# Optimization experiments

Measured on AMD Instinct MI355X. Metric: run time of the kernel, lower is better.

## Reference

```python
import math
import jax, jax.numpy as jnp
import numpy as np

B, L, D = 1, 2048, 3072
H, KV, HD = 32, 32, 96
THETA = 10000.0
MAXP, ORIGP = 131072, 4096
ROPE_SCALE = math.sqrt(1.0 + math.log(MAXP / ORIGP) / math.log(ORIGP))
ATTN_SCALE = HD ** -0.5
OP = H * HD + 2 * KV * HD  # 9216


def setup_inputs() -> dict:
    key = jax.random.key(0)
    k1, k2, k3, k4 = jax.random.split(key, 4)
    return {
        "x": jax.random.normal(k1, (B, L, D), jnp.float32),
        "w_qkv": jax.random.normal(k2, (OP, D), jnp.float32) * (D ** -0.5),
        "w_o": jax.random.normal(k3, (D, H * HD), jnp.float32) * ((H * HD) ** -0.5),
        # Phi-3 su-scaling short factors are ~1.0; sample near 1
        "short_factor": 1.0 + 0.5 * jax.random.uniform(k4, (HD // 2,), jnp.float32),
    }


def _rotate_half(t):
    t1, t2 = jnp.split(t, 2, axis=-1)
    return jnp.concatenate([-t2, t1], axis=-1)


def reference(x, w_qkv, w_o, short_factor):
    # fused QKV projection
    qkv = x @ w_qkv.T  # [B,L,OP]
    q, k, v = jnp.split(qkv, [H * HD, H * HD + KV * HD], axis=-1)
    q = q.reshape(B, L, H, HD).transpose(0, 2, 1, 3)   # [B,H,L,HD]
    k = k.reshape(B, L, KV, HD).transpose(0, 2, 1, 3)  # [B,KV,L,HD]
    v = v.reshape(B, L, KV, HD).transpose(0, 2, 1, 3)

    # SuRoPE (always uses short_factor, matching source)
    pos = jnp.arange(L, dtype=jnp.float32)  # position_ids default arange
    inv_freq = 1.0 / (short_factor * THETA ** (jnp.arange(0, HD, 2, dtype=jnp.float32) / HD))  # [HD/2]
    freqs = pos[:, None] * inv_freq[None, :]            # [L,HD/2]
    emb = jnp.concatenate([freqs, freqs], axis=-1)      # [L,HD]
    cos = (jnp.cos(emb) * ROPE_SCALE)[None, None]       # [1,1,L,HD]
    sin = (jnp.sin(emb) * ROPE_SCALE)[None, None]
    q = q * cos + _rotate_half(q) * sin
    k = k * cos + _rotate_half(k) * sin

    # causal mask, naive attention (matches source)
    mask = jnp.triu(jnp.full((L, L), -jnp.inf, dtype=jnp.float32), 1)
    scores = jnp.einsum('bhqd,bhkd->bhqk', q * ATTN_SCALE, k) + mask
    attn = jax.nn.softmax(scores, axis=-1)
    o = jnp.einsum('bhqk,bhkd->bhqd', attn, v)
    o = o.transpose(0, 2, 1, 3).reshape(B, L, H * HD)
    return o @ w_o.T
```

## Files before the change

kernel.cpp:

```cpp
#include <hip/hip_runtime.h>
#include <math.h>

typedef __attribute__((ext_vector_type(4))) float f32x4;
typedef __attribute__((ext_vector_type(4))) float f4;
typedef __attribute__((ext_vector_type(8))) _Float16 h8;
typedef __attribute__((ext_vector_type(8))) unsigned short us8;

static __device__ __forceinline__ h8 ld8h(const _Float16* p) {
    return __builtin_bit_cast(h8, *(const us8*)p);
}
static __device__ __forceinline__ void glds16(const void* g, void* l) {
    __builtin_amdgcn_global_load_lds((const __attribute__((address_space(1))) unsigned int*)g,
                                     (__attribute__((address_space(3))) unsigned int*)l, 16, 0, 0);
}

__global__ void convert_half(const float* __restrict__ in, _Float16* __restrict__ out, int n8) {
    int i = blockIdx.x * blockDim.x + threadIdx.x;
    if (i >= n8) return;
    f4 v0 = *(const f4*)(in + (size_t)i * 8);
    f4 v1 = *(const f4*)(in + (size_t)i * 8 + 4);
    h8 o;
#pragma unroll
    for (int j = 0; j < 4; j++) {
        o[j] = (_Float16)v0[j];
        o[j + 4] = (_Float16)v1[j];
    }
    *(h8*)(out + (size_t)i * 8) = o;
}

__global__ void rope_table(const float* __restrict__ sf, float* __restrict__ cs,
                           float* __restrict__ sn, float rope_scale) {
    int i = blockIdx.x * blockDim.x + threadIdx.x;
    const int j = i % 48, l = i / 48;
    const float e = (float)(2 * j) / 96.0f;
    const float inv = 1.0f / (sf[j] * powf(10000.0f, e));
    const float ang = (float)l * inv;
    cs[i] = cosf(ang) * rope_scale;
    sn[i] = sinf(ang) * rope_scale;
}

__global__ __launch_bounds__(256, 3) void gemm_qkv(
    const _Float16* __restrict__ A, const _Float16* __restrict__ B,
    const float* __restrict__ cs, const float* __restrict__ sn,
    _Float16* __restrict__ Qh, _Float16* __restrict__ Kh, _Float16* __restrict__ Vh,
    float attn_scale) {
    const int K = 3072;
    __shared__ _Float16 As[2][128][32], Bs[2][192][32];
    const int t = threadIdx.x;
    const int lane = t & 63, w = t >> 6;
    const int bm = blockIdx.y * 128, bn = blockIdx.x * 192;
    const int wm = w >> 1, wn = w & 1;
    const int l15 = lane & 15, l4 = lane >> 4;

    int car[2], cas[2], cbr[3], cbs[3];
#pragma unroll
    for (int i = 0; i < 2; i++) {
        const int c = t + i * 256;
        car[i] = c >> 2;
        cas[i] = (((c & 3) ^ ((car[i] >> 1) & 3)) * 8);
    }
#pragma unroll
    for (int i = 0; i < 3; i++) {
        const int c = t + i * 256;
        cbr[i] = c >> 2;
        cbs[i] = (((c & 3) ^ ((cbr[i] >> 1) & 3)) * 8);
    }

    f32x4 acc[4][6] = {};

#define STG_QKV(k0_, buf)                                                              \
    {                                                                                  \
        _Float16* ab = &As[(buf)][0][0];                                               \
        _Float16* bb = &Bs[(buf)][0][0];                                               \
        _Pragma("unroll") for (int i = 0; i < 2; i++)                                  \
            glds16(A + (size_t)(bm + car[i]) * K + (k0_) + cas[i], ab + (t + i * 256) * 8); \
        _Pragma("unroll") for (int i = 0; i < 3; i++)                                  \
            glds16(B + (size_t)(bn + cbr[i]) * K + (k0_) + cbs[i], bb + (t + i * 256) * 8); \
    }

    STG_QKV(0, 0)

    int cur = 0;
    for (int k0 = 0; k0 < K; k0 += 32) {
        __syncthreads();
        if (k0 + 32 < K) STG_QKV(k0 + 32, cur ^ 1)
        h8 af[4], bf[6];
#pragma unroll
        for (int m = 0; m < 4; m++) {
            const int row = wm * 64 + m * 16 + l15;
            af[m] = ld8h(&As[cur][row][(l4 ^ ((row >> 1) & 3)) * 8]);
        }
#pragma unroll
        for (int n = 0; n < 6; n++) {
            const int row = wn * 96 + n * 16 + l15;
            bf[n] = ld8h(&Bs[cur][row][(l4 ^ ((row >> 1) & 3)) * 8]);
        }
#pragma unroll
        for (int m = 0; m < 4; m++)
#pragma unroll
            for (int n = 0; n < 6; n++)
                acc[m][n] = __builtin_amdgcn_mfma_f32_16x16x32_f16(af[m], bf[n], acc[m][n], 0, 0, 0);
        cur ^= 1;
    }
#undef STG_QKV

    const int opcol0 = bn + wn * 96;
    const int which = opcol0 / 3072;
    const int h = (opcol0 % 3072) / 96;

    if (which == 2) {
#pragma unroll
        for (int m = 0; m < 4; m++)
#pragma unroll
            for (int r = 0; r < 4; r++) {
                const int l = bm + wm * 64 + m * 16 + l4 * 4 + r;
#pragma unroll
                for (int n = 0; n < 6; n++)
                    Vh[((size_t)h * 2048 + l) * 96 + n * 16 + l15] = (_Float16)acc[m][n][r];
            }
    } else {
        _Float16* dst = (which == 0) ? Qh : Kh;
        const float qs = (which == 0) ? attn_scale : 1.0f;
#pragma unroll
        for (int m = 0; m < 4; m++)
#pragma unroll
            for (int r = 0; r < 4; r++) {
                const int l = bm + wm * 64 + m * 16 + l4 * 4 + r;
                const float* csl = cs + l * 48;
                const float* snl = sn + l * 48;
                const size_t rowb = ((size_t)h * 2048 + l) * 96;
#pragma unroll
                for (int n = 0; n < 3; n++) {
                    const int j = n * 16 + l15;
                    const float c = csl[j], s = snl[j];
                    const float lo = acc[m][n][r], hi = acc[m][n + 3][r];
                    dst[rowb + j] = (_Float16)((lo * c - hi * s) * qs);
                    dst[rowb + j + 48] = (_Float16)((hi * c + lo * s) * qs);
                }
            }
    }
}

__global__ __launch_bounds__(256, 3) void gemm_p(
    const _Float16* __restrict__ A, const _Float16* __restrict__ B,
    float* __restrict__ C, int M, int N, int K) {
    __shared__ _Float16 As[2][128][32], Bs[2][96][32];
    const int t = threadIdx.x;
    const int lane = t & 63, w = t >> 6;
    const int bm = blockIdx.y * 128, bn = blockIdx.x * 96;
    const int wy = w >> 1, wx = w & 1;
    const int l15 = lane & 15, l4 = lane >> 4;

    int car[2], cas[2];
#pragma unroll
    for (int i = 0; i < 2; i++) {
        const int c = t + i * 256;
        car[i] = c >> 2;
        cas[i] = (((c & 3) ^ ((car[i] >> 1) & 3)) * 8);
    }
    const int cb0 = t, rb0 = cb0 >> 2, sb0 = (((cb0 & 3) ^ ((rb0 >> 1) & 3)) * 8);
    const int cb1 = t + 256, rb1 = cb1 >> 2, sb1 = (((cb1 & 3) ^ ((rb1 >> 1) & 3)) * 8);
    const bool bex = (t < 128);

    f32x4 acc[4][3] = {};

#define STG_P(k0_, buf)                                                                \
    {                                                                                  \
        _Float16* ab = &As[(buf)][0][0];                                               \
        _Float16* bb = &Bs[(buf)][0][0];                                               \
        _Pragma("unroll") for (int i = 0; i < 2; i++)                                  \
            glds16(A + (size_t)(bm + car[i]) * K + (k0_) + cas[i], ab + (t + i * 256) * 8); \
        glds16(B + (size_t)(bn + rb0) * K + (k0_) + sb0, bb + cb0 * 8);                \
        if (bex) glds16(B + (size_t)(bn + rb1) * K + (k0_) + sb1, bb + cb1 * 8);       \
    }

    STG_P(0, 0)

    int cur = 0;
    for (int k0 = 0; k0 < K; k0 += 32) {
        __syncthreads();
        if (k0 + 32 < K) STG_P(k0 + 32, cur ^ 1)
        h8 af[4], bf[3];
#pragma unroll
        for (int m = 0; m < 4; m++) {
            const int row = wy * 64 + m * 16 + l15;
            af[m] = ld8h(&As[cur][row][(l4 ^ ((row >> 1) & 3)) * 8]);
        }
#pragma unroll
        for (int n = 0; n < 3; n++) {
            const int row = wx * 48 + n * 16 + l15;
            bf[n] = ld8h(&Bs[cur][row][(l4 ^ ((row >> 1) & 3)) * 8]);
        }
#pragma unroll
        for (int m = 0; m < 4; m++)
#pragma unroll
            for (int n = 0; n < 3; n++)
                acc[m][n] = __builtin_amdgcn_mfma_f32_16x16x32_f16(af[m], bf[n], acc[m][n], 0, 0, 0);
        cur ^= 1;
    }
#undef STG_P

#pragma unroll
    for (int m = 0; m < 4; m++)
#pragma unroll
        for (int n = 0; n < 3; n++)
#pragma unroll
            for (int r = 0; r < 4; r++)
                C[(size_t)(bm + wy * 64 + m * 16 + l4 * 4 + r) * N + bn + wx * 48 + n * 16 + l15] =
                    acc[m][n][r];
}

__global__ __launch_bounds__(256) void vtrans(const _Float16* __restrict__ Vh,
                                              _Float16* __restrict__ Vt) {
    __shared__ _Float16 tile[64][105];
    const int h = blockIdx.y;
    const int l0 = blockIdx.x * 64;
    const int t = threadIdx.x;
#pragma unroll
    for (int i = 0; i < 3; i++) {
        const int v = t + i * 256;
        const int row = v / 12, seg = (v % 12) * 8;
        *(us8*)&tile[row][seg] =
            *(const us8*)(Vh + ((size_t)h * 2048 + l0 + row) * 96 + seg);
    }
    __syncthreads();
#pragma unroll
    for (int i = 0; i < 3; i++) {
        const int v = t + i * 256;
        const int d = v >> 3, lc = v & 7;
        h8 o;
#pragma unroll
        for (int j = 0; j < 8; j++) o[j] = tile[lc * 8 + j][d];
        *(h8*)(Vt + ((size_t)h * 96 + d) * 2048 + l0 + lc * 8) = o;
    }
}

__global__ __launch_bounds__(512, 2) void attn_mfma(
    const _Float16* __restrict__ Qh, const _Float16* __restrict__ Kh,
    const _Float16* __restrict__ Vt, _Float16* __restrict__ Oh) {
    __shared__ _Float16 Ks[2][64][104];
    __shared__ _Float16 Vs[2][96][72];
    __shared__ _Float16 Ps[8][16][72];

    const int h = blockIdx.y;
    const int t = threadIdx.x, lane = t & 63, w = t >> 6;
    const int l15 = lane & 15, l4 = lane >> 4;

    const _Float16* Kg = Kh + (size_t)h * 2048 * 96;
    const _Float16* Vg = Vt + (size_t)h * 96 * 2048;

    const int cA = t, rKA = cA / 12, sKA = (cA % 12) * 8;
    const int rVA = cA >> 3, sVA = (cA & 7) * 8;
    const int cB = 512 + t, rKB = cB / 12, sKB = (cB % 12) * 8;
    const int rVB = cB >> 3, sVB = (cB & 7) * 8;
    const bool two = (t < 256);

    for (int ph = 0; ph < 2; ph++) {
        const int qt = ph ? (int)blockIdx.x : 15 - (int)blockIdx.x;
        const int q0 = qt * 128;
        const int wq = q0 + w * 16;

        h8 qf[3];
        const size_t qrow = ((size_t)h * 2048 + wq + l15) * 96;
#pragma unroll
        for (int kc = 0; kc < 3; kc++) qf[kc] = ld8h(Qh + qrow + kc * 32 + l4 * 8);

        us8 kregA, vregA, kregB, vregB;
        kregA = *(const us8*)(Kg + (size_t)rKA * 96 + sKA);
        vregA = *(const us8*)(Vg + (size_t)rVA * 2048 + sVA);
        if (two) {
            kregB = *(const us8*)(Kg + (size_t)rKB * 96 + sKB);
            vregB = *(const us8*)(Vg + (size_t)rVB * 2048 + sVB);
        }

        f32x4 o[6] = {};
        float m_i[4] = {-1e30f, -1e30f, -1e30f, -1e30f};
        float l_i[4] = {0.f, 0.f, 0.f, 0.f};

        const int nkt = 2 * qt + 2;
        for (int kt = 0; kt < nkt; kt++) {
            const int kv0 = kt * 64;
            const int buf = kt & 1;
            *(us8*)&Ks[buf][rKA][sKA] = kregA;
            *(us8*)&Vs[buf][rVA][sVA] = vregA;
            if (two) {
                *(us8*)&Ks[buf][rKB][sKB] = kregB;
                *(us8*)&Vs[buf][rVB][sVB] = vregB;
            }
            __syncthreads();
            if (kt + 1 < nkt) {
                const int kv1 = kv0 + 64;
                kregA = *(const us8*)(Kg + (size_t)(kv1 + rKA) * 96 + sKA);
                vregA = *(const us8*)(Vg + (size_t)rVA * 2048 + kv1 + sVA);
                if (two) {
                    kregB = *(const us8*)(Kg + (size_t)(kv1 + rKB) * 96 + sKB);
                    vregB = *(const us8*)(Vg + (size_t)rVB * 2048 + kv1 + sVB);
                }
            }

            if (kv0 <= wq + 15) {
                f32x4 s[4] = {};
#pragma unroll
                for (int f = 0; f < 4; f++)
#pragma unroll
                    for (int kc = 0; kc < 3; kc++) {
                        h8 kf = ld8h(&Ks[buf][f * 16 + l15][kc * 32 + l4 * 8]);
                        s[f] = __builtin_amdgcn_mfma_f32_16x16x32_f16(qf[kc], kf, s[f], 0, 0, 0);
                    }

                if (kv0 + 63 > wq) {
#pragma unroll
                    for (int f = 0; f < 4; f++)
#pragma unroll
                        for (int r = 0; r < 4; r++)
                            if (kv0 + f * 16 + l15 > wq + l4 * 4 + r) s[f][r] = -1e30f;
                }

                float mx[4];
#pragma unroll
                for (int r = 0; r < 4; r++) {
                    float m0 = fmaxf(fmaxf(s[0][r], s[1][r]), fmaxf(s[2][r], s[3][r]));
#pragma unroll
                    for (int msk = 1; msk < 16; msk <<= 1) m0 = fmaxf(m0, __shfl_xor(m0, msk, 64));
                    mx[r] = m0;
                }

                bool need = false;
#pragma unroll
                for (int r = 0; r < 4; r++) need = need || (mx[r] > m_i[r] + 8.0f);
                if (__any(need)) {
#pragma unroll
                    for (int r = 0; r < 4; r++) {
                        const float mnew = fmaxf(m_i[r], mx[r]);
                        const float sc = __expf(m_i[r] - mnew);
                        m_i[r] = mnew;
                        l_i[r] *= sc;
#pragma unroll
                        for (int f2 = 0; f2 < 6; f2++) o[f2][r] *= sc;
                    }
                }

#pragma unroll
                for (int f = 0; f < 4; f++)
#pragma unroll
                    for (int r = 0; r < 4; r++) {
                        const float p = __expf(s[f][r] - m_i[r]);
                        Ps[w][l4 * 4 + r][f * 16 + l15] = (_Float16)p;
                        l_i[r] += p;
                    }
#pragma unroll
                for (int kc2 = 0; kc2 < 2; kc2++) {
                    h8 pa = ld8h(&Ps[w][l15][kc2 * 32 + l4 * 8]);
#pragma unroll
                    for (int f2 = 0; f2 < 6; f2++) {
                        h8 vb = ld8h(&Vs[buf][f2 * 16 + l15][kc2 * 32 + l4 * 8]);
                        o[f2] = __builtin_amdgcn_mfma_f32_16x16x32_f16(pa, vb, o[f2], 0, 0, 0);
                    }
                }
            }
        }

        __syncthreads();

#pragma unroll
        for (int r = 0; r < 4; r++) {
            float ss = l_i[r];
#pragma unroll
            for (int msk = 1; msk < 16; msk <<= 1) ss += __shfl_xor(ss, msk, 64);
            const float inv = 1.0f / ss;
            const size_t row = (size_t)(wq + l4 * 4 + r) * 3072 + h * 96;
#pragma unroll
            for (int f2 = 0; f2 < 6; f2++)
                Oh[row + f2 * 16 + l15] = (_Float16)(o[f2][r] * inv);
        }
    }
}

extern "C" void kernel_launch(void* const* d_in, const int* in_sizes, int n_in,
                              void* d_out, int out_size, void* d_ws, size_t ws_size,
                              hipStream_t stream) {
    const float* x = (const float*)d_in[0];
    const float* w_qkv = (const float*)d_in[1];
    const float* w_o = (const float*)d_in[2];
    const float* sf = (const float*)d_in[3];
    float* out = (float*)d_out;
    char* ws = (char*)d_ws;

    _Float16* wqkvh = (_Float16*)(ws);
    _Float16* Qh = (_Float16*)(ws + 56623104);
    _Float16* Kh = (_Float16*)(ws + 69206016);
    _Float16* Vh = (_Float16*)(ws + 81788928);
    _Float16* Vth = (_Float16*)(ws + 94371840);
    _Float16* Oh = (_Float16*)(ws + 106954752);
    _Float16* xh = (_Float16*)(ws + 132120576);
    _Float16* woh = (_Float16*)(ws + 144703488);
    float* cs = (float*)(ws + 163577856);
    float* sn = (float*)(ws + 163971072);

    const float rope_scale = (float)sqrt(1.0 + log(131072.0 / 4096.0) / log(4096.0));
    const float attn_scale = (float)(1.0 / sqrt(96.0));

    convert_half<<<3072, 256, 0, stream>>>(x, xh, 786432);
    convert_half<<<13824, 256, 0, stream>>>(w_qkv, wqkvh, 3538944);
    rope_table<<<384, 256, 0, stream>>>(sf, cs, sn, rope_scale);
    gemm_qkv<<<dim3(48, 16), 256, 0, stream>>>(xh, wqkvh, cs, sn, Qh, Kh, Vh, attn_scale);
    vtrans<<<dim3(32, 32), 256, 0, stream>>>(Vh, Vth);
    convert_half<<<4608, 256, 0, stream>>>(w_o, woh, 1179648);
    attn_mfma<<<dim3(8, 32), 512, 0, stream>>>(Qh, Kh, Vth, Oh);
    gemm_p<<<dim3(32, 16), 256, 0, stream>>>(Oh, woh, out, 2048, 3072, 3072);
}
```

Baseline: 317.6 us.

## Process two 16-row query groups per wave in attention, halving block size

The attention kernel now uses 256-thread blocks where each wave owns 32 query rows (two 16-row groups) instead of 16. Each K fragment and V fragment loaded from shared memory is reused for both groups' MFMAs, which cuts LDS reads per MFMA. V fragments are hoisted into registers before the softmax. The cost is more register pressure (two sets of accumulators, scores and Q fragments) and fewer waves per block for latency hiding, with the same total 512 blocks of work arranged over fewer threads.

New measurement: 345.0 us. 1.09x slower.

```diff
diff --git a/kernel.cpp b/kernel.cpp
--- a/kernel.cpp
+++ b/kernel.cpp
@@ -235,12 +235,12 @@
     }
 }
 
-__global__ __launch_bounds__(512, 2) void attn_mfma(
+__global__ __launch_bounds__(256, 2) void attn_mfma(
     const _Float16* __restrict__ Qh, const _Float16* __restrict__ Kh,
     const _Float16* __restrict__ Vt, _Float16* __restrict__ Oh) {
     __shared__ _Float16 Ks[2][64][104];
     __shared__ _Float16 Vs[2][96][72];
-    __shared__ _Float16 Ps[8][16][72];
+    __shared__ _Float16 Ps[4][16][72];
 
     const int h = blockIdx.y;
     const int t = threadIdx.x, lane = t & 63, w = t >> 6;
@@ -249,130 +249,155 @@
     const _Float16* Kg = Kh + (size_t)h * 2048 * 96;
     const _Float16* Vg = Vt + (size_t)h * 96 * 2048;
 
-    const int cA = t, rKA = cA / 12, sKA = (cA % 12) * 8;
-    const int rVA = cA >> 3, sVA = (cA & 7) * 8;
-    const int cB = 512 + t, rKB = cB / 12, sKB = (cB % 12) * 8;
-    const int rVB = cB >> 3, sVB = (cB & 7) * 8;
-    const bool two = (t < 256);
+    int rK[3], sK[3], rV[3], sV[3];
+#pragma unroll
+    for (int i = 0; i < 3; i++) {
+        const int c = t + i * 256;
+        rK[i] = c / 12; sK[i] = (c % 12) * 8;
+        rV[i] = c >> 3; sV[i] = (c & 7) * 8;
+    }
 
     for (int ph = 0; ph < 2; ph++) {
         const int qt = ph ? (int)blockIdx.x : 15 - (int)blockIdx.x;
         const int q0 = qt * 128;
-        const int wq = q0 + w * 16;
-
-        h8 qf[3];
-        const size_t qrow = ((size_t)h * 2048 + wq + l15) * 96;
-#pragma unroll
-        for (int kc = 0; kc < 3; kc++) qf[kc] = ld8h(Qh + qrow + kc * 32 + l4 * 8);
-
-        us8 kregA, vregA, kregB, vregB;
-        kregA = *(const us8*)(Kg + (size_t)rKA * 96 + sKA);
-        vregA = *(const us8*)(Vg + (size_t)rVA * 2048 + sVA);
-        if (two) {
-            kregB = *(const us8*)(Kg + (size_t)rKB * 96 + sKB);
-            vregB = *(const us8*)(Vg + (size_t)rVB * 2048 + sVB);
-        }
-
-        f32x4 o[6] = {};
-        float m_i[4] = {-1e30f, -1e30f, -1e30f, -1e30f};
-        float l_i[4] = {0.f, 0.f, 0.f, 0.f};
+        const int wq = q0 + w * 32;
+
+        h8 qf[2][3];
+#pragma unroll
+        for (int g = 0; g < 2; g++) {
+            const size_t qrow = ((size_t)h * 2048 + wq + g * 16 + l15) * 96;
+#pragma unroll
+            for (int kc = 0; kc < 3; kc++) qf[g][kc] = ld8h(Qh + qrow + kc * 32 + l4 * 8);
+        }
+
+        us8 kreg[3], vreg[3];
+#pragma unroll
+        for (int i = 0; i < 3; i++) {
+            kreg[i] = *(const us8*)(Kg + (size_t)rK[i] * 96 + sK[i]);
+            vreg[i] = *(const us8*)(Vg + (size_t)rV[i] * 2048 + sV[i]);
+        }
+
+        f32x4 o[2][6] = {};
+        float m_i[2][4], l_i[2][4];
+#pragma unroll
+        for (int g = 0; g < 2; g++)
+#pragma unroll
+            for (int r = 0; r < 4; r++) { m_i[g][r] = -1e30f; l_i[g][r] = 0.f; }
 
         const int nkt = 2 * qt + 2;
         for (int kt = 0; kt < nkt; kt++) {
             const int kv0 = kt * 64;
             const int buf = kt & 1;
-            *(us8*)&Ks[buf][rKA][sKA] = kregA;
-            *(us8*)&Vs[buf][rVA][sVA] = vregA;
-            if (two) {
-                *(us8*)&Ks[buf][rKB][sKB] = kregB;
-                *(us8*)&Vs[buf][rVB][sVB] = vregB;
+#pragma unroll
+            for (int i = 0; i < 3; i++) {
+                *(us8*)&Ks[buf][rK[i]][sK[i]] = kreg[i];
+                *(us8*)&Vs[buf][rV[i]][sV[i]] = vreg[i];
             }
             __syncthreads();
             if (kt + 1 < nkt) {
                 const int kv1 = kv0 + 64;
-                kregA = *(const us8*)(Kg + (size_t)(kv1 + rKA) * 96 + sKA);
-                vregA = *(const us8*)(Vg + (size_t)rVA * 2048 + kv1 + sVA);
-                if (two) {
-                    kregB = *(const us8*)(Kg + (size_t)(kv1 + rKB) * 96 + sKB);
-                    vregB = *(const us8*)(Vg + (size_t)rVB * 2048 + kv1 + sVB);
+#pragma unroll
+                for (int i = 0; i < 3; i++) {
+                    kreg[i] = *(const us8*)(Kg + (size_t)(kv1 + rK[i]) * 96 + sK[i]);
+                    vreg[i] = *(const us8*)(Vg + (size_t)rV[i] * 2048 + kv1 + sV[i]);
                 }
             }
 
-            if (kv0 <= wq + 15) {
-                f32x4 s[4] = {};
+            if (kv0 <= wq + 31) {
+                f32x4 s[2][4] = {};
 #pragma unroll
                 for (int f = 0; f < 4; f++)
 #pragma unroll
                     for (int kc = 0; kc < 3; kc++) {
                         h8 kf = ld8h(&Ks[buf][f * 16 + l15][kc * 32 + l4 * 8]);
-                        s[f] = __builtin_amdgcn_mfma_f32_16x16x32_f16(qf[kc], kf, s[f], 0, 0, 0);
+#pragma unroll
+                        for (int g = 0; g < 2; g++)
+                            s[g][f] = __builtin_amdgcn_mfma_f32_16x16x32_f16(qf[g][kc], kf, s[g][f], 0, 0, 0);
                     }
 
                 if (kv0 + 63 > wq) {
 #pragma unroll
+                    for (int g = 0; g < 2; g++)
+#pragma unroll
+                        for (int f = 0; f < 4; f++)
+#pragma unroll
+                            for (int r = 0; r < 4; r++)
+                                if (kv0 + f * 16 + l15 > wq + g * 16 + l4 * 4 + r) s[g][f][r] = -1e30f;
+                }
+
+                h8 vb[2][6];
+#pragma unroll
+                for (int kc2 = 0; kc2 < 2; kc2++)
+#pragma unroll
+                    for (int f2 = 0; f2 < 6; f2++)
+                        vb[kc2][f2] = ld8h(&Vs[buf][f2 * 16 + l15][kc2 * 32 + l4 * 8]);
+
+                float mx[2][4];
+#pragma unroll
+                for (int g = 0; g < 2; g++)
+#pragma unroll
+                    for (int r = 0; r < 4; r++) {
+                        float m0 = fmaxf(fmaxf(s[g][0][r], s[g][1][r]), fmaxf(s[g][2][r], s[g][3][r]));
+#pragma unroll
+                        for (int msk = 1; msk < 16; msk <<= 1) m0 = fmaxf(m0, __shfl_xor(m0, msk, 64));
+                        mx[g][r] = m0;
+                    }
+
+                bool need = false;
+#pragma unroll
+                for (int g = 0; g < 2; g++)
+#pragma unroll
+                    for (int r = 0; r < 4; r++) need = need || (mx[g][r] > m_i[g][r] + 8.0f);
+                if (__any(need)) {
+#pragma unroll
+                    for (int g = 0; g < 2; g++)
+#pragma unroll
+                        for (int r = 0; r < 4; r++) {
+                            const float mnew = fmaxf(m_i[g][r], mx[g][r]);
+                            const float sc = __expf(m_i[g][r] - mnew);
+                            m_i[g][r] = mnew;
+                            l_i[g][r] *= sc;
+#pragma unroll
+                            for (int f2 = 0; f2 < 6; f2++) o[g][f2][r] *= sc;
+                        }
+                }
+
+#pragma unroll
+                for (int g = 0; g < 2; g++) {
+#pragma unroll
                     for (int f = 0; f < 4; f++)
 #pragma unroll
-                        for (int r = 0; r < 4; r++)
-                            if (kv0 + f * 16 + l15 > wq + l4 * 4 + r) s[f][r] = -1e30f;
-                }
-
-                float mx[4];
-#pragma unroll
-                for (int r = 0; r < 4; r++) {
-                    float m0 = fmaxf(fmaxf(s[0][r], s[1][r]), fmaxf(s[2][r], s[3][r]));
-#pragma unroll
-                    for (int msk = 1; msk < 16; msk <<= 1) m0 = fmaxf(m0, __shfl_xor(m0, msk, 64));
-                    mx[r] = m0;
-                }
-
-                bool need = false;
-#pragma unroll
-                for (int r = 0; r < 4; r++) need = need || (mx[r] > m_i[r] + 8.0f);
-                if (__any(need)) {
-#pragma unroll
-                    for (int r = 0; r < 4; r++) {
-                        const float mnew = fmaxf(m_i[r], mx[r]);
-                        const float sc = __expf(m_i[r] - mnew);
-                        m_i[r] = mnew;
-                        l_i[r] *= sc;
-#pragma unroll
-                        for (int f2 = 0; f2 < 6; f2++) o[f2][r] *= sc;
+                        for (int r = 0; r < 4; r++) {
+                            const float p = __expf(s[g][f][r] - m_i[g][r]);
+                            Ps[w][l4 * 4 + r][f * 16 + l15] = (_Float16)p;
+                            l_i[g][r] += p;
+                        }
+#pragma unroll
+                    for (int kc2 = 0; kc2 < 2; kc2++) {
+                        h8 pa = ld8h(&Ps[w][l15][kc2 * 32 + l4 * 8]);
+#pragma unroll
+                        for (int f2 = 0; f2 < 6; f2++)
+                            o[g][f2] = __builtin_amdgcn_mfma_f32_16x16x32_f16(pa, vb[kc2][f2], o[g][f2], 0, 0, 0);
                     }
                 }
-
-#pragma unroll
-                for (int f = 0; f < 4; f++)
-#pragma unroll
-                    for (int r = 0; r < 4; r++) {
-                        const float p = __expf(s[f][r] - m_i[r]);
-                        Ps[w][l4 * 4 + r][f * 16 + l15] = (_Float16)p;
-                        l_i[r] += p;
-                    }
-#pragma unroll
-                for (int kc2 = 0; kc2 < 2; kc2++) {
-                    h8 pa = ld8h(&Ps[w][l15][kc2 * 32 + l4 * 8]);
-#pragma unroll
-                    for (int f2 = 0; f2 < 6; f2++) {
-                        h8 vb = ld8h(&Vs[buf][f2 * 16 + l15][kc2 * 32 + l4 * 8]);
-                        o[f2] = __builtin_amdgcn_mfma_f32_16x16x32_f16(pa, vb, o[f2], 0, 0, 0);
-                    }
-                }
             }
         }
 
         __syncthreads();
 
 #pragma unroll
-        for (int r = 0; r < 4; r++) {
-            float ss = l_i[r];
-#pragma unroll
-            for (int msk = 1; msk < 16; msk <<= 1) ss += __shfl_xor(ss, msk, 64);
-            const float inv = 1.0f / ss;
-            const size_t row = (size_t)(wq + l4 * 4 + r) * 3072 + h * 96;
-#pragma unroll
-            for (int f2 = 0; f2 < 6; f2++)
-                Oh[row + f2 * 16 + l15] = (_Float16)(o[f2][r] * inv);
-        }
+        for (int g = 0; g < 2; g++)
+#pragma unroll
+            for (int r = 0; r < 4; r++) {
+                float ss = l_i[g][r];
+#pragma unroll
+                for (int msk = 1; msk < 16; msk <<= 1) ss += __shfl_xor(ss, msk, 64);
+                const float inv = 1.0f / ss;
+                const size_t row = (size_t)(wq + g * 16 + l4 * 4 + r) * 3072 + h * 96;
+#pragma unroll
+                for (int f2 = 0; f2 < 6; f2++)
+                    Oh[row + f2 * 16 + l15] = (_Float16)(o[g][f2][r] * inv);
+            }
     }
 }
 
@@ -406,6 +431,6 @@
     gemm_qkv<<<dim3(48, 16), 256, 0, stream>>>(xh, wqkvh, cs, sn, Qh, Kh, Vh, attn_scale);
     vtrans<<<dim3(32, 32), 256, 0, stream>>>(Vh, Vth);
     convert_half<<<4608, 256, 0, stream>>>(w_o, woh, 1179648);
-    attn_mfma<<<dim3(8, 32), 512, 0, stream>>>(Qh, Kh, Vth, Oh);
+    attn_mfma<<<dim3(8, 32), 256, 0, stream>>>(Qh, Kh, Vth, Oh);
     gemm_p<<<dim3(32, 16), 256, 0, stream>>>(Oh, woh, out, 2048, 3072, 3072);
 }
```
